# Kernel optimization log

Hardware: AMD Instinct MI355X
Metric: run time of the kernel (lower is better)

## Reference

```python
import jax, jax.numpy as jnp
import numpy as np

B, T, F = 32, 512, 300      # batch, seq_len, raw feature columns
S, KMAX = 256, 32           # number of active slots, max thresholds per slot


def setup_inputs() -> dict:
    key = jax.random.key(0)
    k1, k2, k3 = jax.random.split(key, 3)
    # ragged bucket counts in [8, 32]
    bucket_nums = (8 + (jnp.arange(S) % 25)).astype(jnp.int32)
    # sorted per-slot thresholds in [0,1], padded with +inf past bucket_num
    raw = jnp.sort(jax.random.uniform(k1, (S, KMAX), dtype=jnp.float32), axis=-1)
    valid = jnp.arange(KMAX)[None, :] < bucket_nums[:, None]
    thresholds = jnp.where(valid, raw, jnp.inf)
    slot_ids = jax.random.randint(k2, (S,), 0, F, dtype=jnp.int32)
    features = jax.random.uniform(k3, (B, T, F), dtype=jnp.float32)
    return {"features": features, "thresholds": thresholds,
            "slot_ids": slot_ids, "bucket_nums": bucket_nums}


def reference(features, thresholds, slot_ids, bucket_nums):
    # gather the per-slot feature columns: [B, T, S]
    vals = features[:, :, slot_ids]
    # validity mask over padded threshold axis: [S, KMAX]
    valid = jnp.arange(KMAX, dtype=bucket_nums.dtype)[None, :] < bucket_nums[:, None]
    # torch.lt(one_slot.unsqueeze(-1), threshold): [B, T, S, KMAX]
    cmp = (vals[..., None] < thresholds[None, None]) & valid[None, None]
    is_hit = jnp.any(cmp, axis=-1)                       # [B, T, S]
    # weights bucket_num..1 over valid entries, 0 on padding -> argmax picks
    # the FIRST true comparison, exactly like the torch arange(bn,0,-1) trick
    weights = jnp.where(valid,
                        bucket_nums[:, None] - jnp.arange(KMAX, dtype=bucket_nums.dtype)[None, :],
                        0)                               # [S, KMAX]
    tmp = cmp.astype(jnp.int32) * weights[None, None]    # [B, T, S, KMAX]
    indices = jnp.argmax(tmp, axis=-1).astype(jnp.int32) # [B, T, S]
    # misses map to bucket_num (out-of-range bucket)
    out = jnp.where(is_hit, indices, bucket_nums[None, None, :])
    return out
```

## Files before the change

kernel.cpp:

```cpp
#include <hip/hip_runtime.h>

constexpr int B = 32, T = 512, F = 300, S = 256, KMAX = 32;
constexpr int T_PER_BLOCK = 16;

__global__ __launch_bounds__(256, 4) void SequenceBucketPreprocessor_kernel(
    const float* __restrict__ features,
    const float* __restrict__ thresholds,
    const int*   __restrict__ slot_ids,
    int*         __restrict__ out)
{
    __shared__ float lds[T_PER_BLOCK * F];

    const int s   = threadIdx.x;
    const int bt0 = blockIdx.x * T_PER_BLOCK;

    constexpr int NCHUNK = T_PER_BLOCK * F / 4;
    const float4* gsrc = reinterpret_cast<const float4*>(features + bt0 * F);
    float4*       ldst = reinterpret_cast<float4*>(lds);
    #pragma unroll
    for (int r = 0; r < (NCHUNK + S - 1) / S; ++r) {
        const int i = r * S + s;
        if (i < NCHUNK) ldst[i] = gsrc[i];
    }

    float thr[KMAX];
    const float4* trow = reinterpret_cast<const float4*>(thresholds + s * KMAX);
    #pragma unroll
    for (int q = 0; q < KMAX / 4; ++q) {
        float4 v = trow[q];
        thr[q * 4 + 0] = v.x;
        thr[q * 4 + 1] = v.y;
        thr[q * 4 + 2] = v.z;
        thr[q * 4 + 3] = v.w;
    }
    const int slot = slot_ids[s];

    __syncthreads();

    #pragma unroll
    for (int j0 = 0; j0 < T_PER_BLOCK; j0 += 8) {
        float v[8];
        #pragma unroll
        for (int j = 0; j < 8; ++j)
            v[j] = lds[(j0 + j) * F + slot];

        int c[8] = {0, 0, 0, 0, 0, 0, 0, 0};
        #pragma unroll
        for (int k = 0; k < KMAX; ++k) {
            #pragma unroll
            for (int j = 0; j < 8; ++j)
                c[j] += (thr[k] <= v[j]);
        }

        #pragma unroll
        for (int j = 0; j < 8; ++j)
            out[(bt0 + j0 + j) * S + s] = c[j];
    }
}

extern "C" void kernel_launch(void* const* d_in, const int* in_sizes, int n_in,
                              void* d_out, int out_size, void* d_ws, size_t ws_size,
                              hipStream_t stream) {
    const float* features   = (const float*)d_in[0];
    const float* thresholds = (const float*)d_in[1];
    const int*   slot_ids   = (const int*)d_in[2];
    int* out = (int*)d_out;

    const int n_bt   = B * T;
    const int blocks = n_bt / T_PER_BLOCK;
    SequenceBucketPreprocessor_kernel<<<dim3(blocks), dim3(S), 0, stream>>>(
        features, thresholds, slot_ids, out);
}
```

Baseline: 84.85 us.

## Gather slot features directly from global memory instead of staging rows in LDS

Drops the cooperative float4 copy of the full 16x300 feature tile into shared memory and the barrier after it. Each thread now gathers its 16 slot values straight from global memory, relying on L1/L2 caching, and then processes all 16 rows in a single pass. Output stores become nontemporal. This cuts LDS traffic and synchronisation and may raise occupancy, but it replaces coalesced vector loads with scattered 4-byte gathers and adds register pressure.

```diff
diff --git a/kernel.cpp b/kernel.cpp
--- a/kernel.cpp
+++ b/kernel.cpp
@@ -9,53 +9,41 @@
     const int*   __restrict__ slot_ids,
     int*         __restrict__ out)
 {
-    __shared__ float lds[T_PER_BLOCK * F];
-
     const int s   = threadIdx.x;
     const int bt0 = blockIdx.x * T_PER_BLOCK;
-
-    constexpr int NCHUNK = T_PER_BLOCK * F / 4;
-    const float4* gsrc = reinterpret_cast<const float4*>(features + bt0 * F);
-    float4*       ldst = reinterpret_cast<float4*>(lds);
-    #pragma unroll
-    for (int r = 0; r < (NCHUNK + S - 1) / S; ++r) {
-        const int i = r * S + s;
-        if (i < NCHUNK) ldst[i] = gsrc[i];
-    }
 
     float thr[KMAX];
     const float4* trow = reinterpret_cast<const float4*>(thresholds + s * KMAX);
     #pragma unroll
     for (int q = 0; q < KMAX / 4; ++q) {
-        float4 v = trow[q];
-        thr[q * 4 + 0] = v.x;
-        thr[q * 4 + 1] = v.y;
-        thr[q * 4 + 2] = v.z;
-        thr[q * 4 + 3] = v.w;
+        float4 t4 = trow[q];
+        thr[q * 4 + 0] = t4.x;
+        thr[q * 4 + 1] = t4.y;
+        thr[q * 4 + 2] = t4.z;
+        thr[q * 4 + 3] = t4.w;
     }
     const int slot = slot_ids[s];
 
-    __syncthreads();
+    float v[T_PER_BLOCK];
+    const float* fbase = features + (long)bt0 * F + slot;
+    #pragma unroll
+    for (int j = 0; j < T_PER_BLOCK; ++j)
+        v[j] = fbase[j * F];
+
+    int c[T_PER_BLOCK];
+    #pragma unroll
+    for (int j = 0; j < T_PER_BLOCK; ++j) c[j] = 0;
 
     #pragma unroll
-    for (int j0 = 0; j0 < T_PER_BLOCK; j0 += 8) {
-        float v[8];
+    for (int k = 0; k < KMAX; ++k) {
         #pragma unroll
-        for (int j = 0; j < 8; ++j)
-            v[j] = lds[(j0 + j) * F + slot];
+        for (int j = 0; j < T_PER_BLOCK; ++j)
+            c[j] += (thr[k] <= v[j]);
+    }
 
-        int c[8] = {0, 0, 0, 0, 0, 0, 0, 0};
-        #pragma unroll
-        for (int k = 0; k < KMAX; ++k) {
-            #pragma unroll
-            for (int j = 0; j < 8; ++j)
-                c[j] += (thr[k] <= v[j]);
-        }
-
-        #pragma unroll
-        for (int j = 0; j < 8; ++j)
-            out[(bt0 + j0 + j) * S + s] = c[j];
-    }
+    #pragma unroll
+    for (int j = 0; j < T_PER_BLOCK; ++j)
+        __builtin_nontemporal_store(c[j], out + (bt0 + j) * S + s);
 }
 
 extern "C" void kernel_launch(void* const* d_in, const int* in_sizes, int n_in,
```

After: 81.35 us. 4.1% less time.
